# Kernel optimization log

Measured on AMD Instinct MI355X. Metric: run time of the kernel, lower is better.

The kernel has to match this reference:

```python
import jax, jax.numpy as jnp
import numpy as np

B, D, E, H, DEPTH, NH, K = 4, 384, 8, 1536, 12, 6, 2
P, NTOK = 16, 197  # patch size, 14*14 patches + cls
EPS = 1e-6


def layernorm(x, w, b):
    m = x.mean(-1, keepdims=True)
    v = ((x - m) ** 2).mean(-1, keepdims=True)
    return (x - m) / jnp.sqrt(v + EPS) * w + b


def attention(x, qkv_w, qkv_b, proj_w, proj_b):
    Bn, N, C = x.shape
    hd = C // NH
    qkv = x @ qkv_w.T + qkv_b                       # [B,N,3C]
    qkv = qkv.reshape(Bn, N, 3, NH, hd).transpose(2, 0, 3, 1, 4)
    q, k, v = qkv[0], qkv[1], qkv[2]                # [B,h,N,hd]
    attn = jax.nn.softmax((q @ k.transpose(0, 1, 3, 2)) * (hd ** -0.5), axis=-1)
    out = (attn @ v).transpose(0, 2, 1, 3).reshape(Bn, N, C)
    return out @ proj_w.T + proj_b


def mlp(x, w1, b1, w2, b2):
    h = jax.nn.gelu(x @ w1.T + b1, approximate=False)
    return h @ w2.T + b2


def moe_ffn(x2d, gw, w1, b1, w2, b2):
    # noiseless top-k gating (eval mode of NoisyTopKGating)
    logits = x2d @ gw                                # [T,E]
    T = logits.shape[0]
    top_vals, top_idx = jax.lax.top_k(logits, K + 1)
    gates_k = jax.nn.softmax(top_vals[:, :K], axis=-1)
    gates = jnp.zeros((T, E), x2d.dtype).at[jnp.arange(T)[:, None], top_idx[:, :K]].set(gates_k)
    # dense per-expert FFN, weighted combine (identical math to SparseDispatcher)
    h = jax.nn.gelu(jnp.einsum('td,edh->teh', x2d, w1) + b1, approximate=False)
    out = jnp.einsum('teh,ehd->ted', h, w2) + b2
    return jnp.einsum('te,ted->td', gates, out)


def forward(x, patch_w, patch_b, cls_token, pos_embed,
            ln1_w, ln1_b, qkv_w, qkv_b, proj_w, proj_b, ln2_w, ln2_b,
            fc1_w, fc1_b, fc2_w, fc2_b,
            gate_w, moe_w1, moe_b1, moe_w2, moe_b2, lnf_w, lnf_b):
    # patch embed: conv k=16 s=16
    feat = jax.lax.conv_general_dilated(x, patch_w, (P, P), 'VALID',
                                        dimension_numbers=('NCHW', 'OIHW', 'NCHW'))
    feat = feat + patch_b[None, :, None, None]
    Bn = feat.shape[0]
    tokens = feat.reshape(Bn, D, -1).transpose(0, 2, 1)          # [B,196,D]
    cls = jnp.broadcast_to(cls_token, (Bn, 1, D))
    h = jnp.concatenate([cls, tokens], axis=1) + pos_embed       # [B,197,D]

    for i in range(DEPTH):
        h = h + attention(layernorm(h, ln1_w[i], ln1_b[i]), qkv_w[i], qkv_b[i], proj_w[i], proj_b[i])
        y = layernorm(h, ln2_w[i], ln2_b[i])
        if i % 2 == 1:
            j = i // 2
            y2 = moe_ffn(y.reshape(-1, D), gate_w[j], moe_w1[j], moe_b1[j], moe_w2[j], moe_b2[j])
            h = h + y2.reshape(Bn, NTOK, D)
        else:
            j = i // 2
            h = h + mlp(y, fc1_w[j], fc1_b[j], fc2_w[j], fc2_b[j])
    return layernorm(h, lnf_w, lnf_b)


def setup_inputs() -> dict:
    key = jax.random.key(0)
    ks = jax.random.split(key, 16)
    rn = lambda k, s, sd=0.02: jax.random.normal(k, s, jnp.float32) * sd
    return {
        'x': jax.random.normal(ks[0], (B, 3, 224, 224), jnp.float32),
        'patch_w': rn(ks[1], (D, 3, P, P)), 'patch_b': jnp.zeros((D,), jnp.float32),
        'cls_token': rn(ks[2], (1, 1, D)), 'pos_embed': rn(ks[3], (1, NTOK, D)),
        'ln1_w': jnp.ones((DEPTH, D), jnp.float32), 'ln1_b': jnp.zeros((DEPTH, D), jnp.float32),
        'qkv_w': rn(ks[4], (DEPTH, 3 * D, D)), 'qkv_b': jnp.zeros((DEPTH, 3 * D), jnp.float32),
        'proj_w': rn(ks[5], (DEPTH, D, D)), 'proj_b': jnp.zeros((DEPTH, D), jnp.float32),
        'ln2_w': jnp.ones((DEPTH, D), jnp.float32), 'ln2_b': jnp.zeros((DEPTH, D), jnp.float32),
        'fc1_w': rn(ks[6], (DEPTH // 2, H, D)), 'fc1_b': jnp.zeros((DEPTH // 2, H), jnp.float32),
        'fc2_w': rn(ks[7], (DEPTH // 2, D, H)), 'fc2_b': jnp.zeros((DEPTH // 2, D), jnp.float32),
        'gate_w': rn(ks[8], (DEPTH // 2, D, E)),
        'moe_w1': rn(ks[9], (DEPTH // 2, E, D, H)), 'moe_b1': jnp.zeros((DEPTH // 2, E, H), jnp.float32),
        'moe_w2': rn(ks[10], (DEPTH // 2, E, H, D)), 'moe_b2': jnp.zeros((DEPTH // 2, E, D), jnp.float32),
        'lnf_w': jnp.ones((D,), jnp.float32), 'lnf_b': jnp.zeros((D,), jnp.float32),
    }


def reference(x, patch_w, patch_b, cls_token, pos_embed,
              ln1_w, ln1_b, qkv_w, qkv_b, proj_w, proj_b, ln2_w, ln2_b,
              fc1_w, fc1_b, fc2_w, fc2_b,
              gate_w, moe_w1, moe_b1, moe_w2, moe_b2, lnf_w, lnf_b):
    return forward(x, patch_w, patch_b, cls_token, pos_embed,
                   ln1_w, ln1_b, qkv_w, qkv_b, proj_w, proj_b, ln2_w, ln2_b,
                   fc1_w, fc1_b, fc2_w, fc2_b,
                   gate_w, moe_w1, moe_b1, moe_w2, moe_b2, lnf_w, lnf_b)
```

## Files before the change

kernel.cpp:

```cpp
#include <hip/hip_runtime.h>
#include <math.h>

#define NBATCH 4
#define NTOK 197
#define TT 788
#define DM 384
#define HM 1536
#define NHEAD 6
#define NEXP 8
#define LD2 72
#define MOUTSZ (TT * 2 * DM)

typedef __attribute__((ext_vector_type(8))) short bf16x8;
typedef __attribute__((ext_vector_type(4))) float f32x4;

__device__ __forceinline__ void f2bf2(float x, short& hi, short& lo) {
    unsigned u = __float_as_uint(x);
    unsigned uh = u + (0x7fffu + ((u >> 16) & 1u));
    hi = (short)(uh >> 16);
    float hf = __uint_as_float(uh & 0xffff0000u);
    float r = x - hf;
    unsigned v = __float_as_uint(r);
    lo = (short)((v + (0x7fffu + ((v >> 16) & 1u))) >> 16);
}
__device__ __forceinline__ float gelu_f(float x) {
    return 0.5f * x * (1.0f + erff(x * 0.7071067811865475f));
}

__global__ void k_im2col(const float* __restrict__ X, float* __restrict__ P) {
    int p = blockIdx.x;
    int b = p / 196, pp = p % 196;
    int py = pp / 14, px = pp % 14;
    const float* xb = X + (size_t)b * 3 * 224 * 224;
    float* dst = P + (size_t)p * 768;
    for (int idx = threadIdx.x; idx < 768; idx += 256) {
        int c = idx >> 8;
        int i = (idx >> 4) & 15;
        int j = idx & 15;
        dst[idx] = xb[((size_t)c * 224 + py * 16 + i) * 224 + px * 16 + j];
    }
}

__global__ void k_assemble(const float* __restrict__ PO, const float* __restrict__ pb,
                           const float* __restrict__ cls, const float* __restrict__ pos,
                           float* __restrict__ H) {
    int t = blockIdx.x;
    int b = t / NTOK, n = t % NTOK;
    for (int d = threadIdx.x; d < DM; d += 128) {
        float v;
        if (n == 0) v = cls[d];
        else v = PO[((size_t)b * 196 + (n - 1)) * DM + d] + pb[d];
        H[(size_t)t * DM + d] = v + pos[(size_t)n * DM + d];
    }
}

__global__ void k_ln(const float* __restrict__ X, const float* __restrict__ w,
                     const float* __restrict__ b, float* __restrict__ Y) {
    int t = blockIdx.x, lane = threadIdx.x;
    const float* x = X + (size_t)t * DM;
    float v[6];
    float s = 0.f;
    #pragma unroll
    for (int i = 0; i < 6; ++i) { v[i] = x[lane + i * 64]; s += v[i]; }
    #pragma unroll
    for (int off = 32; off; off >>= 1) s += __shfl_xor(s, off);
    float mean = s * (1.f / 384.f);
    float q = 0.f;
    #pragma unroll
    for (int i = 0; i < 6; ++i) { float d = v[i] - mean; q += d * d; }
    #pragma unroll
    for (int off = 32; off; off >>= 1) q += __shfl_xor(q, off);
    float inv = rsqrtf(q * (1.f / 384.f) + 1e-6f);
    float* y = Y + (size_t)t * DM;
    #pragma unroll
    for (int i = 0; i < 6; ++i) {
        int d = lane + i * 64;
        y[d] = (v[i] - mean) * inv * w[d] + b[d];
    }
}

__global__ __launch_bounds__(256) void k_gemm_mfma(
    const float* __restrict__ A, const float* __restrict__ W,
    const float* __restrict__ bias, float* __restrict__ C,
    int M, int N, int K, int flags, int MT, int NT, int wprot, int ksplit,
    const float* __restrict__ lnw, const float* __restrict__ lnb)
{
    int mt, nt, ks = 0;
    {
        int lane8 = blockIdx.x & 7;
        int idx = blockIdx.x >> 3;
        if (ksplit > 1) { ks = idx % ksplit; idx /= ksplit; }
        if (wprot) {
            mt = idx % MT;
            nt = lane8 + 8 * (idx / MT);
            if (nt >= NT) return;
        } else {
            nt = idx % NT;
            mt = lane8 + 8 * (idx / NT);
            if (mt >= MT) return;
        }
    }
    const int Ks = K / ksplit;
    const float* Ab = A + (size_t)ks * Ks;
    const float* Wb = W + (size_t)ks * Ks;
    __shared__ short Ah[64 * LD2], Al[64 * LD2], Bh[64 * LD2], Bl[64 * LD2];
    const int bm = mt * 64, bn = nt * 64;
    const int tid = threadIdx.x;
    const int lane = tid & 63, w = tid >> 6;
    const int wr = w >> 1, wc = w & 1;
    const int r16 = lane & 15, g = lane >> 4;
    const int sr = tid >> 4;
    const int sc = (tid & 15) * 4;
    const bool doln = (flags & 8) != 0;
    float am[4], ai[4];
    #pragma unroll
    for (int p = 0; p < 4; ++p) { am[p] = 0.f; ai[p] = 1.f; }
    if (doln) {
        int j = tid & 15;
        #pragma unroll
        for (int p = 0; p < 4; ++p) {
            int r = bm + sr + p * 16;
            if (r < M) {
                const float* xr = A + (size_t)r * K;
                float s = 0.f, ss = 0.f;
                #pragma unroll
                for (int i = 0; i < 6; ++i) {
                    float4 v = *(const float4*)(xr + j * 4 + i * 64);
                    s += v.x + v.y + v.z + v.w;
                    ss += v.x * v.x + v.y * v.y + v.z * v.z + v.w * v.w;
                }
                #pragma unroll
                for (int off = 1; off < 16; off <<= 1) {
                    s += __shfl_xor(s, off);
                    ss += __shfl_xor(ss, off);
                }
                float mean = s * (1.f / 384.f);
                float var = ss * (1.f / 384.f) - mean * mean;
                am[p] = mean;
                ai[p] = rsqrtf(var + 1e-6f);
            }
        }
    }
    float4 ra[4], rb[4], lw4, lb4;
    auto LOADT = [&](int k0) {
        if (doln) {
            lw4 = *(const float4*)(lnw + k0 + sc);
            lb4 = *(const float4*)(lnb + k0 + sc);
        }
        #pragma unroll
        for (int p = 0; p < 4; ++p) {
            int r = sr + p * 16;
            ra[p] = make_float4(0.f, 0.f, 0.f, 0.f);
            if (bm + r < M) ra[p] = *(const float4*)(Ab + (size_t)(bm + r) * K + k0 + sc);
            rb[p] = *(const float4*)(Wb + (size_t)(bn + r) * K + k0 + sc);
        }
    };
    auto STORET = [&]() {
        #pragma unroll
        for (int p = 0; p < 4; ++p) {
            int r = sr + p * 16;
            float4 a4 = ra[p];
            if (doln) {
                a4.x = (a4.x - am[p]) * ai[p] * lw4.x + lb4.x;
                a4.y = (a4.y - am[p]) * ai[p] * lw4.y + lb4.y;
                a4.z = (a4.z - am[p]) * ai[p] * lw4.z + lb4.z;
                a4.w = (a4.w - am[p]) * ai[p] * lw4.w + lb4.w;
            }
            float4 b4 = rb[p];
            short4 ah, al, bh, bl;
            f2bf2(a4.x, ah.x, al.x); f2bf2(a4.y, ah.y, al.y);
            f2bf2(a4.z, ah.z, al.z); f2bf2(a4.w, ah.w, al.w);
            f2bf2(b4.x, bh.x, bl.x); f2bf2(b4.y, bh.y, bl.y);
            f2bf2(b4.z, bh.z, bl.z); f2bf2(b4.w, bh.w, bl.w);
            *(short4*)&Ah[r * LD2 + sc] = ah; *(short4*)&Al[r * LD2 + sc] = al;
            *(short4*)&Bh[r * LD2 + sc] = bh; *(short4*)&Bl[r * LD2 + sc] = bl;
        }
    };
    f32x4 acc[2][2] = {};
    auto COMPUTE = [&]() {
        #pragma unroll
        for (int kk = 0; kk < 2; ++kk) {
            bf16x8 afh[2], afl[2], bfh[2], bfl[2];
            #pragma unroll
            for (int i = 0; i < 2; ++i) {
                int off = (wr * 32 + i * 16 + r16) * LD2 + kk * 32 + g * 8;
                afh[i] = *(const bf16x8*)&Ah[off];
                afl[i] = *(const bf16x8*)&Al[off];
            }
            #pragma unroll
            for (int j = 0; j < 2; ++j) {
                int off = (wc * 32 + j * 16 + r16) * LD2 + kk * 32 + g * 8;
                bfh[j] = *(const bf16x8*)&Bh[off];
                bfl[j] = *(const bf16x8*)&Bl[off];
            }
            #pragma unroll
            for (int i = 0; i < 2; ++i)
                #pragma unroll
                for (int j = 0; j < 2; ++j) {
                    acc[i][j] = __builtin_amdgcn_mfma_f32_16x16x32_bf16(afl[i], bfh[j], acc[i][j], 0, 0, 0);
                    acc[i][j] = __builtin_amdgcn_mfma_f32_16x16x32_bf16(afh[i], bfl[j], acc[i][j], 0, 0, 0);
                    acc[i][j] = __builtin_amdgcn_mfma_f32_16x16x32_bf16(afh[i], bfh[j], acc[i][j], 0, 0, 0);
                }
        }
    };
    LOADT(0);
    STORET();
    __syncthreads();
    for (int k0 = 64; k0 < Ks; k0 += 64) {
        LOADT(k0);
        COMPUTE();
        __syncthreads();
        STORET();
        __syncthreads();
    }
    COMPUTE();
    #pragma unroll
    for (int i = 0; i < 2; ++i) {
        #pragma unroll
        for (int j = 0; j < 2; ++j) {
            int n = bn + wc * 32 + j * 16 + r16;
            float bb = (bias && ks == 0) ? bias[n] : 0.f;
            int mbase = bm + wr * 32 + i * 16 + g * 4;
            #pragma unroll
            for (int r = 0; r < 4; ++r) {
                int m = mbase + r;
                if (m < M) {
                    float v = acc[i][j][r] + bb;
                    float* cp = C + (size_t)m * N + n;
                    if (flags & 16) {
                        atomicAdd(cp, v);
                    } else {
                        if (flags & 1) v = gelu_f(v);
                        if (flags & 2) v += *cp;
                        *cp = v;
                    }
                }
            }
        }
    }
}

__global__ __launch_bounds__(256) void k_gemm32(
    const float* __restrict__ A, const float* __restrict__ W,
    const float* __restrict__ bias, float* __restrict__ C,
    int M, int N, int K, int flags, int MT, int NT,
    const float* __restrict__ lnw, const float* __restrict__ lnb)
{
    int mt, nt;
    {
        int lane8 = blockIdx.x & 7;
        int idx = blockIdx.x >> 3;
        mt = idx % MT;
        nt = lane8 + 8 * (idx / MT);
        if (nt >= NT) return;
    }
    __shared__ short Ah[32 * LD2], Al[32 * LD2], Bh[64 * LD2], Bl[64 * LD2];
    const int bm = mt * 32, bn = nt * 64;
    const int tid = threadIdx.x;
    const int lane = tid & 63, w = tid >> 6;
    const int r16 = lane & 15, g = lane >> 4;
    const int sa = tid >> 3;
    const int ja = tid & 7;
    const int sca = ja * 8;
    const int sr = tid >> 4;
    const int sc = (tid & 15) * 4;
    const bool doln = (flags & 8) != 0;
    const bool dogelu = (flags & 1) != 0;
    const int rowA = bm + sa;
    const bool aok = rowA < M;
    float am = 0.f, ai = 1.f;
    if (doln && aok) {
        const float* xr = A + (size_t)rowA * K;
        float s = 0.f, ss = 0.f;
        #pragma unroll
        for (int i = 0; i < 12; ++i) {
            float4 v = *(const float4*)(xr + ja * 48 + i * 4);
            s += v.x + v.y + v.z + v.w;
            ss += v.x * v.x + v.y * v.y + v.z * v.z + v.w * v.w;
        }
        #pragma unroll
        for (int off = 1; off < 8; off <<= 1) {
            s += __shfl_xor(s, off);
            ss += __shfl_xor(ss, off);
        }
        float mean = s * (1.f / 384.f);
        float var = ss * (1.f / 384.f) - mean * mean;
        am = mean;
        ai = rsqrtf(var + 1e-6f);
    }
    float4 ra0, ra1, rb[4], lwa0, lwa1, lba0, lba1;
    auto LOADT = [&](int k0) {
        if (doln) {
            lwa0 = *(const float4*)(lnw + k0 + sca);
            lwa1 = *(const float4*)(lnw + k0 + sca + 4);
            lba0 = *(const float4*)(lnb + k0 + sca);
            lba1 = *(const float4*)(lnb + k0 + sca + 4);
        }
        ra0 = make_float4(0.f, 0.f, 0.f, 0.f);
        ra1 = ra0;
        if (aok) {
            ra0 = *(const float4*)(A + (size_t)rowA * K + k0 + sca);
            ra1 = *(const float4*)(A + (size_t)rowA * K + k0 + sca + 4);
        }
        #pragma unroll
        for (int p = 0; p < 4; ++p) {
            int r = sr + p * 16;
            rb[p] = *(const float4*)(W + (size_t)(bn + r) * K + k0 + sc);
        }
    };
    auto STORET = [&]() {
        float4 a0 = ra0, a1 = ra1;
        if (doln) {
            a0.x = (a0.x - am) * ai * lwa0.x + lba0.x;
            a0.y = (a0.y - am) * ai * lwa0.y + lba0.y;
            a0.z = (a0.z - am) * ai * lwa0.z + lba0.z;
            a0.w = (a0.w - am) * ai * lwa0.w + lba0.w;
            a1.x = (a1.x - am) * ai * lwa1.x + lba1.x;
            a1.y = (a1.y - am) * ai * lwa1.y + lba1.y;
            a1.z = (a1.z - am) * ai * lwa1.z + lba1.z;
            a1.w = (a1.w - am) * ai * lwa1.w + lba1.w;
        }
        short4 h0, l0, h1, l1;
        f2bf2(a0.x, h0.x, l0.x); f2bf2(a0.y, h0.y, l0.y);
        f2bf2(a0.z, h0.z, l0.z); f2bf2(a0.w, h0.w, l0.w);
        f2bf2(a1.x, h1.x, l1.x); f2bf2(a1.y, h1.y, l1.y);
        f2bf2(a1.z, h1.z, l1.z); f2bf2(a1.w, h1.w, l1.w);
        *(short4*)&Ah[sa * LD2 + sca] = h0; *(short4*)&Ah[sa * LD2 + sca + 4] = h1;
        *(short4*)&Al[sa * LD2 + sca] = l0; *(short4*)&Al[sa * LD2 + sca + 4] = l1;
        #pragma unroll
        for (int p = 0; p < 4; ++p) {
            int r = sr + p * 16;
            float4 b4 = rb[p];
            short4 bh, bl;
            f2bf2(b4.x, bh.x, bl.x); f2bf2(b4.y, bh.y, bl.y);
            f2bf2(b4.z, bh.z, bl.z); f2bf2(b4.w, bh.w, bl.w);
            *(short4*)&Bh[r * LD2 + sc] = bh; *(short4*)&Bl[r * LD2 + sc] = bl;
        }
    };
    f32x4 acc[2] = {};
    auto COMPUTE = [&]() {
        #pragma unroll
        for (int kk = 0; kk < 2; ++kk) {
            bf16x8 afh[2], afl[2], bfh, bfl;
            #pragma unroll
            for (int i = 0; i < 2; ++i) {
                int off = (i * 16 + r16) * LD2 + kk * 32 + g * 8;
                afh[i] = *(const bf16x8*)&Ah[off];
                afl[i] = *(const bf16x8*)&Al[off];
            }
            {
                int off = (w * 16 + r16) * LD2 + kk * 32 + g * 8;
                bfh = *(const bf16x8*)&Bh[off];
                bfl = *(const bf16x8*)&Bl[off];
            }
            #pragma unroll
            for (int i = 0; i < 2; ++i) {
                acc[i] = __builtin_amdgcn_mfma_f32_16x16x32_bf16(afl[i], bfh, acc[i], 0, 0, 0);
                acc[i] = __builtin_amdgcn_mfma_f32_16x16x32_bf16(afh[i], bfl, acc[i], 0, 0, 0);
                acc[i] = __builtin_amdgcn_mfma_f32_16x16x32_bf16(afh[i], bfh, acc[i], 0, 0, 0);
            }
        }
    };
    LOADT(0);
    STORET();
    __syncthreads();
    for (int k0 = 64; k0 < K; k0 += 64) {
        LOADT(k0);
        COMPUTE();
        __syncthreads();
        STORET();
        __syncthreads();
    }
    COMPUTE();
    #pragma unroll
    for (int i = 0; i < 2; ++i) {
        int n = bn + w * 16 + r16;
        float bb = bias ? bias[n] : 0.f;
        int mbase = bm + i * 16 + g * 4;
        #pragma unroll
        for (int r = 0; r < 4; ++r) {
            int m = mbase + r;
            if (m < M) {
                float v = acc[i][r] + bb;
                if (dogelu) v = gelu_f(v);
                C[(size_t)m * N + n] = v;
            }
        }
    }
}

__global__ __launch_bounds__(256) void k_scoresm(const float* __restrict__ QKV,
                                                 float* __restrict__ S) {
    int z = blockIdx.y;
    int b = z / NHEAD, hh = z % NHEAD;
    int i0 = blockIdx.x * 32;
    __shared__ float qs[32][65];
    __shared__ float ks[32][65];
    __shared__ float srow[32][200];
    int tid = threadIdx.x;
    int r = tid >> 3, d0 = (tid & 7) * 8, c0 = (tid & 7) * 4, l8 = tid & 7;
    {
        float4 v0 = make_float4(0,0,0,0), v1 = v0;
        if (i0 + r < NTOK) {
            const float* qp = QKV + ((size_t)(b * NTOK + i0 + r)) * 1152 + hh * 64 + d0;
            v0 = *(const float4*)qp; v1 = *(const float4*)(qp + 4);
        }
        qs[r][d0+0]=v0.x; qs[r][d0+1]=v0.y; qs[r][d0+2]=v0.z; qs[r][d0+3]=v0.w;
        qs[r][d0+4]=v1.x; qs[r][d0+5]=v1.y; qs[r][d0+6]=v1.z; qs[r][d0+7]=v1.w;
    }
    if (l8 == 0) { srow[r][197] = -1e30f; srow[r][198] = -1e30f; srow[r][199] = -1e30f; }
    for (int j0 = 0; j0 < NTOK; j0 += 32) {
        __syncthreads();
        {
            float4 v0 = make_float4(0,0,0,0), v1 = v0;
            if (j0 + r < NTOK) {
                const float* kp = QKV + ((size_t)(b * NTOK + j0 + r)) * 1152 + 384 + hh * 64 + d0;
                v0 = *(const float4*)kp; v1 = *(const float4*)(kp + 4);
            }
            ks[r][d0+0]=v0.x; ks[r][d0+1]=v0.y; ks[r][d0+2]=v0.z; ks[r][d0+3]=v0.w;
            ks[r][d0+4]=v1.x; ks[r][d0+5]=v1.y; ks[r][d0+6]=v1.z; ks[r][d0+7]=v1.w;
        }
        __syncthreads();
        float acc[4] = {0.f, 0.f, 0.f, 0.f};
        #pragma unroll 8
        for (int d = 0; d < 64; ++d) {
            float qv = qs[r][d];
            #pragma unroll
            for (int u = 0; u < 4; ++u) acc[u] += qv * ks[c0 + u][d];
        }
        #pragma unroll
        for (int u = 0; u < 4; ++u) {
            int j = j0 + c0 + u;
            if (j < NTOK) srow[r][j] = acc[u] * 0.125f;
        }
    }
    __syncthreads();
    float m = -1e30f;
    for (int c = l8; c < 200; c += 8) m = fmaxf(m, srow[r][c]);
    #pragma unroll
    for (int off = 1; off < 8; off <<= 1) m = fmaxf(m, __shfl_xor(m, off));
    float s = 0.f;
    for (int c = l8; c < 200; c += 8) {
        float e = expf(srow[r][c] - m);
        srow[r][c] = e;
        s += e;
    }
    #pragma unroll
    for (int off = 1; off < 8; off <<= 1) s += __shfl_xor(s, off);
    float invs = 1.f / s;
    int i = i0 + r;
    if (i < NTOK) {
        float* sp = S + ((size_t)z * NTOK + i) * NTOK;
        for (int c = l8; c < NTOK; c += 8) sp[c] = srow[r][c] * invs;
    }
}

__global__ __launch_bounds__(256) void k_pv(const float* __restrict__ S, const float* __restrict__ QKV,
                                            float* __restrict__ AO) {
    int z = blockIdx.y;
    int b = z / NHEAD, hh = z % NHEAD;
    int i0 = blockIdx.x * 32;
    __shared__ float ps[32][33];
    __shared__ float vs[32][65];
    int tid = threadIdx.x;
    int r = tid >> 3;
    int c4 = (tid & 7) * 4;
    int d0 = (tid & 7) * 8;
    float acc[8] = {};
    for (int k0 = 0; k0 < NTOK; k0 += 32) {
        #pragma unroll
        for (int u = 0; u < 4; ++u) {
            int i = i0 + r, j = k0 + c4 + u;
            ps[r][c4 + u] = (i < NTOK && j < NTOK) ? S[((size_t)z * NTOK + i) * NTOK + j] : 0.f;
        }
        {
            float4 v0 = make_float4(0,0,0,0), v1 = v0;
            if (k0 + r < NTOK) {
                const float* vp = QKV + ((size_t)(b * NTOK + k0 + r)) * 1152 + 768 + hh * 64 + d0;
                v0 = *(const float4*)vp; v1 = *(const float4*)(vp + 4);
            }
            vs[r][d0+0]=v0.x; vs[r][d0+1]=v0.y; vs[r][d0+2]=v0.z; vs[r][d0+3]=v0.w;
            vs[r][d0+4]=v1.x; vs[r][d0+5]=v1.y; vs[r][d0+6]=v1.z; vs[r][d0+7]=v1.w;
        }
        __syncthreads();
        #pragma unroll 8
        for (int kk = 0; kk < 32; ++kk) {
            float pw = ps[r][kk];
            #pragma unroll
            for (int j = 0; j < 8; ++j) acc[j] += pw * vs[kk][d0 + j];
        }
        __syncthreads();
    }
    int i = i0 + r;
    if (i < NTOK) {
        float* op = AO + (size_t)(b * NTOK + i) * DM + hh * 64 + d0;
        #pragma unroll
        for (int j = 0; j < 8; ++j) op[j] = acc[j];
    }
}

__global__ void k_route_ln(const float* __restrict__ H, float* __restrict__ lnstat,
                           const float* __restrict__ lnw, const float* __restrict__ lnb,
                           const float* __restrict__ GW,
                           int* __restrict__ eidx, float* __restrict__ egate) {
    int t = blockIdx.x * 4 + (threadIdx.x >> 6);
    if (t >= TT) return;
    int lane = threadIdx.x & 63;
    const float* x = H + (size_t)t * DM;
    float v[6];
    float s = 0.f, ss = 0.f;
    #pragma unroll
    for (int i = 0; i < 6; ++i) {
        v[i] = x[lane + i * 64];
        s += v[i];
        ss += v[i] * v[i];
    }
    #pragma unroll
    for (int off = 32; off; off >>= 1) { s += __shfl_xor(s, off); ss += __shfl_xor(ss, off); }
    float mean = s * (1.f / 384.f);
    float var = ss * (1.f / 384.f) - mean * mean;
    float inv = rsqrtf(var + 1e-6f);
    if (lane == 0) { lnstat[2 * t] = mean; lnstat[2 * t + 1] = inv; }
    float l8v[NEXP] = {};
    #pragma unroll
    for (int i = 0; i < 6; ++i) {
        int d = lane + i * 64;
        float yv = (v[i] - mean) * inv * lnw[d] + lnb[d];
        const float* g = GW + (size_t)d * NEXP;
        #pragma unroll
        for (int e = 0; e < NEXP; ++e) l8v[e] += yv * g[e];
    }
    #pragma unroll
    for (int e = 0; e < NEXP; ++e) {
        float vv = l8v[e];
        #pragma unroll
        for (int off = 32; off; off >>= 1) vv += __shfl_xor(vv, off);
        l8v[e] = vv;
    }
    if (lane == 0) {
        int b0 = 0;
        #pragma unroll
        for (int e = 1; e < NEXP; ++e) if (l8v[e] > l8v[b0]) b0 = e;
        int b1 = -1;
        #pragma unroll
        for (int e = 0; e < NEXP; ++e) if (e != b0 && (b1 < 0 || l8v[e] > l8v[b1])) b1 = e;
        float e1 = expf(l8v[b1] - l8v[b0]);
        float denom = 1.f + e1;
        eidx[2 * t] = b0; eidx[2 * t + 1] = b1;
        egate[2 * t] = 1.f / denom; egate[2 * t + 1] = e1 / denom;
    }
}

__global__ void k_pscatter(int* __restrict__ cnt, int* __restrict__ basep,
                           const int* __restrict__ eidx,
                           int* __restrict__ slot_tok, int* __restrict__ slot_of) {
    __shared__ int hist[NEXP];
    __shared__ int bp[NEXP];
    __shared__ int fl[NEXP];
    int tid = threadIdx.x;
    if (tid < NEXP) { hist[tid] = 0; fl[tid] = 0; }
    __syncthreads();
    for (int i = tid; i < 2 * TT; i += 256) atomicAdd(&hist[eidx[i]], 1);
    __syncthreads();
    if (tid == 0) {
        int s = 0;
        for (int e = 0; e < NEXP; ++e) { bp[e] = s; s += hist[e]; }
    }
    __syncthreads();
    if (tid < NEXP) { cnt[tid] = hist[tid]; basep[tid] = bp[tid]; }
    for (int t = tid; t < TT; t += 256) {
        #pragma unroll
        for (int k = 0; k < 2; ++k) {
            int e = eidx[2 * t + k];
            int pos = atomicAdd(&fl[e], 1);
            int s = bp[e] + pos;
            slot_tok[s] = t;
            slot_of[2 * t + k] = s;
        }
    }
}

__global__ __launch_bounds__(256) void k_moe1_mfma(
    const float* __restrict__ H, const float* __restrict__ lnstat,
    const float* __restrict__ lnw, const float* __restrict__ lnb,
    const float* __restrict__ W1, const float* __restrict__ B1,
    const int* __restrict__ slot_tok, const int* __restrict__ cnt, const int* __restrict__ basep,
    float* __restrict__ HID)
{
    const int e = blockIdx.x & 7;
    const int idx = blockIdx.x >> 3;
    const int mt = idx % 13;
    const int nt = idx / 13;
    const int c = cnt[e];
    const int r0 = mt * 64;
    if (r0 >= c) return;
    const int sbase = basep[e];
    const int n0 = nt * 64;
    const float* W = W1 + (size_t)e * DM * HM;
    const float* B1e = B1 + (size_t)e * HM;
    __shared__ short Ah[64 * LD2], Al[64 * LD2], Bh[64 * LD2], Bl[64 * LD2];
    const int tid = threadIdx.x;
    const int lane = tid & 63, w = tid >> 6;
    const int wr = w >> 1, wc = w & 1;
    const int r16 = lane & 15, g = lane >> 4;
    const int sr = tid >> 4, sc = (tid & 15) * 4;
    const int kq = (tid >> 4) * 4;
    int tokp[4];
    float am4[4], ai4[4];
    #pragma unroll
    for (int p = 0; p < 4; ++p) {
        int m = r0 + sr + p * 16;
        tokp[p] = (m < c) ? slot_tok[sbase + m] : -1;
        am4[p] = 0.f; ai4[p] = 1.f;
        if (tokp[p] >= 0) { am4[p] = lnstat[2 * tokp[p]]; ai4[p] = lnstat[2 * tokp[p] + 1]; }
    }
    f32x4 acc[2][2] = {};
    for (int k0 = 0; k0 < DM; k0 += 64) {
        float4 lw4 = *(const float4*)(lnw + k0 + sc);
        float4 lb4 = *(const float4*)(lnb + k0 + sc);
        #pragma unroll
        for (int p = 0; p < 4; ++p) {
            int r = sr + p * 16;
            float4 a4 = make_float4(0.f, 0.f, 0.f, 0.f);
            if (tokp[p] >= 0) {
                a4 = *(const float4*)(H + (size_t)tokp[p] * DM + k0 + sc);
                a4.x = (a4.x - am4[p]) * ai4[p] * lw4.x + lb4.x;
                a4.y = (a4.y - am4[p]) * ai4[p] * lw4.y + lb4.y;
                a4.z = (a4.z - am4[p]) * ai4[p] * lw4.z + lb4.z;
                a4.w = (a4.w - am4[p]) * ai4[p] * lw4.w + lb4.w;
            }
            short4 ah, al;
            f2bf2(a4.x, ah.x, al.x); f2bf2(a4.y, ah.y, al.y);
            f2bf2(a4.z, ah.z, al.z); f2bf2(a4.w, ah.w, al.w);
            *(short4*)&Ah[r * LD2 + sc] = ah; *(short4*)&Al[r * LD2 + sc] = al;
        }
        {
            float4 b4[4];
            #pragma unroll
            for (int i = 0; i < 4; ++i)
                b4[i] = *(const float4*)(W + (size_t)(k0 + kq + i) * HM + n0 + sc);
            float col[4][4] = {
                { b4[0].x, b4[1].x, b4[2].x, b4[3].x },
                { b4[0].y, b4[1].y, b4[2].y, b4[3].y },
                { b4[0].z, b4[1].z, b4[2].z, b4[3].z },
                { b4[0].w, b4[1].w, b4[2].w, b4[3].w } };
            #pragma unroll
            for (int u = 0; u < 4; ++u) {
                short4 hh, ll;
                f2bf2(col[u][0], hh.x, ll.x); f2bf2(col[u][1], hh.y, ll.y);
                f2bf2(col[u][2], hh.z, ll.z); f2bf2(col[u][3], hh.w, ll.w);
                *(short4*)&Bh[(sc + u) * LD2 + kq] = hh;
                *(short4*)&Bl[(sc + u) * LD2 + kq] = ll;
            }
        }
        __syncthreads();
        #pragma unroll
        for (int kk = 0; kk < 2; ++kk) {
            bf16x8 afh[2], afl[2], bfh[2], bfl[2];
            #pragma unroll
            for (int i = 0; i < 2; ++i) {
                int off = (wr * 32 + i * 16 + r16) * LD2 + kk * 32 + g * 8;
                afh[i] = *(const bf16x8*)&Ah[off];
                afl[i] = *(const bf16x8*)&Al[off];
            }
            #pragma unroll
            for (int j = 0; j < 2; ++j) {
                int off = (wc * 32 + j * 16 + r16) * LD2 + kk * 32 + g * 8;
                bfh[j] = *(const bf16x8*)&Bh[off];
                bfl[j] = *(const bf16x8*)&Bl[off];
            }
            #pragma unroll
            for (int i = 0; i < 2; ++i)
                #pragma unroll
                for (int j = 0; j < 2; ++j) {
                    acc[i][j] = __builtin_amdgcn_mfma_f32_16x16x32_bf16(afl[i], bfh[j], acc[i][j], 0, 0, 0);
                    acc[i][j] = __builtin_amdgcn_mfma_f32_16x16x32_bf16(afh[i], bfl[j], acc[i][j], 0, 0, 0);
                    acc[i][j] = __builtin_amdgcn_mfma_f32_16x16x32_bf16(afh[i], bfh[j], acc[i][j], 0, 0, 0);
                }
        }
        __syncthreads();
    }
    #pragma unroll
    for (int i = 0; i < 2; ++i) {
        #pragma unroll
        for (int j = 0; j < 2; ++j) {
            int n = n0 + wc * 32 + j * 16 + r16;
            float bb = B1e[n];
            #pragma unroll
            for (int r = 0; r < 4; ++r) {
                int m = r0 + wr * 32 + i * 16 + g * 4 + r;
                if (m < c)
                    HID[(size_t)(sbase + m) * HM + n] = gelu_f(acc[i][j][r] + bb);
            }
        }
    }
}

__global__ __launch_bounds__(256) void k_moe2_mfma(
    const float* __restrict__ HID, const float* __restrict__ W2,
    const int* __restrict__ cnt, const int* __restrict__ basep,
    float* __restrict__ MOUTP)
{
    const int e = blockIdx.x & 7;
    const int idx = blockIdx.x >> 3;
    const int mt = idx % 13;
    const int rest = idx / 13;
    const int nt = rest % 6;
    const int ks = rest / 6;
    const int c = cnt[e];
    const int r0 = mt * 64;
    if (r0 >= c) return;
    const int sbase = basep[e];
    const int n0 = nt * 64;
    const int kbase = ks * 384;
    const float* W = W2 + (size_t)e * HM * DM + (size_t)kbase * DM;
    float* outp = MOUTP + (size_t)ks * MOUTSZ;
    __shared__ short Ah[64 * LD2], Al[64 * LD2], Bh[64 * LD2], Bl[64 * LD2];
    const int tid = threadIdx.x;
    const int lane = tid & 63, w = tid >> 6;
    const int wr = w >> 1, wc = w & 1;
    const int r16 = lane & 15, g = lane >> 4;
    const int sr = tid >> 4, sc = (tid & 15) * 4;
    const int kq = (tid >> 4) * 4;
    f32x4 acc[2][2] = {};
    for (int k0 = 0; k0 < 384; k0 += 64) {
        #pragma unroll
        for (int p = 0; p < 4; ++p) {
            int r = sr + p * 16;
            int m = r0 + r;
            float4 a4 = make_float4(0.f, 0.f, 0.f, 0.f);
            if (m < c) a4 = *(const float4*)(HID + (size_t)(sbase + m) * HM + kbase + k0 + sc);
            short4 ah, al;
            f2bf2(a4.x, ah.x, al.x); f2bf2(a4.y, ah.y, al.y);
            f2bf2(a4.z, ah.z, al.z); f2bf2(a4.w, ah.w, al.w);
            *(short4*)&Ah[r * LD2 + sc] = ah; *(short4*)&Al[r * LD2 + sc] = al;
        }
        {
            float4 b4[4];
            #pragma unroll
            for (int i = 0; i < 4; ++i)
                b4[i] = *(const float4*)(W + (size_t)(k0 + kq + i) * DM + n0 + sc);
            float col[4][4] = {
                { b4[0].x, b4[1].x, b4[2].x, b4[3].x },
                { b4[0].y, b4[1].y, b4[2].y, b4[3].y },
                { b4[0].z, b4[1].z, b4[2].z, b4[3].z },
                { b4[0].w, b4[1].w, b4[2].w, b4[3].w } };
            #pragma unroll
            for (int u = 0; u < 4; ++u) {
                short4 hh, ll;
                f2bf2(col[u][0], hh.x, ll.x); f2bf2(col[u][1], hh.y, ll.y);
                f2bf2(col[u][2], hh.z, ll.z); f2bf2(col[u][3], hh.w, ll.w);
                *(short4*)&Bh[(sc + u) * LD2 + kq] = hh;
                *(short4*)&Bl[(sc + u) * LD2 + kq] = ll;
            }
        }
        __syncthreads();
        #pragma unroll
        for (int kk = 0; kk < 2; ++kk) {
            bf16x8 afh[2], afl[2], bfh[2], bfl[2];
            #pragma unroll
            for (int i = 0; i < 2; ++i) {
                int off = (wr * 32 + i * 16 + r16) * LD2 + kk * 32 + g * 8;
                afh[i] = *(const bf16x8*)&Ah[off];
                afl[i] = *(const bf16x8*)&Al[off];
            }
            #pragma unroll
            for (int j = 0; j < 2; ++j) {
                int off = (wc * 32 + j * 16 + r16) * LD2 + kk * 32 + g * 8;
                bfh[j] = *(const bf16x8*)&Bh[off];
                bfl[j] = *(const bf16x8*)&Bl[off];
            }
            #pragma unroll
            for (int i = 0; i < 2; ++i)
                #pragma unroll
                for (int j = 0; j < 2; ++j) {
                    acc[i][j] = __builtin_amdgcn_mfma_f32_16x16x32_bf16(afl[i], bfh[j], acc[i][j], 0, 0, 0);
                    acc[i][j] = __builtin_amdgcn_mfma_f32_16x16x32_bf16(afh[i], bfl[j], acc[i][j], 0, 0, 0);
                    acc[i][j] = __builtin_amdgcn_mfma_f32_16x16x32_bf16(afh[i], bfh[j], acc[i][j], 0, 0, 0);
                }
        }
        __syncthreads();
    }
    #pragma unroll
    for (int i = 0; i < 2; ++i) {
        #pragma unroll
        for (int j = 0; j < 2; ++j) {
            int n = n0 + wc * 32 + j * 16 + r16;
            #pragma unroll
            for (int r = 0; r < 4; ++r) {
                int m = r0 + wr * 32 + i * 16 + g * 4 + r;
                if (m < c)
                    outp[(size_t)(sbase + m) * DM + n] = acc[i][j][r];
            }
        }
    }
}

__global__ void k_combine(const float* __restrict__ MOUTP, const int* __restrict__ slot_of,
                          const int* __restrict__ eidx, const float* __restrict__ egate,
                          const float* __restrict__ B2, float* __restrict__ H) {
    int t = blockIdx.x;
    int s0 = slot_of[2 * t], s1 = slot_of[2 * t + 1];
    int e0 = eidx[2 * t], e1 = eidx[2 * t + 1];
    float g0 = egate[2 * t], g1 = egate[2 * t + 1];
    for (int d = threadIdx.x; d < DM; d += 128) {
        float v0 = B2[(size_t)e0 * DM + d];
        float v1 = B2[(size_t)e1 * DM + d];
        #pragma unroll
        for (int p = 0; p < 4; ++p) {
            v0 += MOUTP[(size_t)p * MOUTSZ + (size_t)s0 * DM + d];
            v1 += MOUTP[(size_t)p * MOUTSZ + (size_t)s1 * DM + d];
        }
        H[(size_t)t * DM + d] += g0 * v0 + g1 * v1;
    }
}

extern "C" void kernel_launch(void* const* d_in, const int* in_sizes, int n_in,
                              void* d_out, int out_size, void* d_ws, size_t ws_size,
                              hipStream_t stream) {
    const float* x         = (const float*)d_in[0];
    const float* patch_w   = (const float*)d_in[1];
    const float* patch_b   = (const float*)d_in[2];
    const float* cls_token = (const float*)d_in[3];
    const float* pos_embed = (const float*)d_in[4];
    const float* ln1_w     = (const float*)d_in[5];
    const float* ln1_b     = (const float*)d_in[6];
    const float* qkv_w     = (const float*)d_in[7];
    const float* qkv_b     = (const float*)d_in[8];
    const float* proj_w    = (const float*)d_in[9];
    const float* proj_b    = (const float*)d_in[10];
    const float* ln2_w     = (const float*)d_in[11];
    const float* ln2_b     = (const float*)d_in[12];
    const float* fc1_w     = (const float*)d_in[13];
    const float* fc1_b     = (const float*)d_in[14];
    const float* fc2_w     = (const float*)d_in[15];
    const float* fc2_b     = (const float*)d_in[16];
    const float* gate_w    = (const float*)d_in[17];
    const float* moe_w1    = (const float*)d_in[18];
    const float* moe_b1    = (const float*)d_in[19];
    const float* moe_w2    = (const float*)d_in[20];
    const float* moe_b2    = (const float*)d_in[21];
    const float* lnf_w     = (const float*)d_in[22];
    const float* lnf_b     = (const float*)d_in[23];
    float* out = (float*)d_out;

    float* wsf = (float*)d_ws;
    float* regA     = wsf;
    float* patches  = regA;
    float* patchout = regA + 602112;
    float* moehid   = regA;
    float* h     = regA + 2420736;
    float* spare = h + 302592;
    float* qkvb  = spare + 302592;
    float* attno = qkvb + 907776;
    float* regC  = attno + 302592;
    float* S    = regC;
    float* hid  = regC;
    float* mout4 = qkvb;
    float* egate = regC + 1210368;
    int* ib       = (int*)(egate + 1576);
    int* eidx     = ib;
    int* slot_tok = ib + 1576;
    int* slot_of  = ib + 3152;
    int* cnt      = ib + 4728;
    int* basep    = ib + 4736;
    float* lnstat = (float*)(ib + 4752);

    k_im2col<<<784, 256, 0, stream>>>(x, patches);
    k_gemm_mfma<<<96, 256, 0, stream>>>(patches, patch_w, nullptr, patchout,
                                        784, DM, 768, 0, 13, 6, 0, 1, nullptr, nullptr);
    k_assemble<<<TT, 128, 0, stream>>>(patchout, patch_b, cls_token, pos_embed, h);

    for (int l = 0; l < 12; ++l) {
        k_gemm32<<<600, 256, 0, stream>>>(h, qkv_w + (size_t)l * 1152 * DM,
                                          qkv_b + l * 1152, qkvb, TT, 1152, DM, 8,
                                          25, 18, ln1_w + l * DM, ln1_b + l * DM);
        k_scoresm<<<dim3(7, NBATCH * NHEAD), 256, 0, stream>>>(qkvb, S);
        k_pv<<<dim3(7, NBATCH * NHEAD), 256, 0, stream>>>(S, qkvb, attno);
        k_gemm_mfma<<<192, 256, 0, stream>>>(attno, proj_w + (size_t)l * DM * DM,
                                             proj_b + l * DM, h, TT, DM, DM, 16,
                                             13, 6, 0, 2, nullptr, nullptr);
        int j = l >> 1;
        if ((l & 1) == 0) {
            k_gemm32<<<600, 256, 0, stream>>>(h, fc1_w + (size_t)j * HM * DM,
                                              fc1_b + j * HM, hid, TT, HM, DM, 9,
                                              25, 24, ln2_w + l * DM, ln2_b + l * DM);
            k_gemm_mfma<<<384, 256, 0, stream>>>(hid, fc2_w + (size_t)j * DM * HM,
                                                 fc2_b + j * DM, h, TT, DM, HM, 16,
                                                 13, 6, 0, 4, nullptr, nullptr);
        } else {
            k_route_ln<<<197, 256, 0, stream>>>(h, lnstat, ln2_w + l * DM, ln2_b + l * DM,
                                                gate_w + (size_t)j * DM * NEXP, eidx, egate);
            k_pscatter<<<1, 256, 0, stream>>>(cnt, basep, eidx, slot_tok, slot_of);
            k_moe1_mfma<<<8 * 13 * 24, 256, 0, stream>>>(
                h, lnstat, ln2_w + l * DM, ln2_b + l * DM,
                moe_w1 + (size_t)j * NEXP * DM * HM, moe_b1 + (size_t)j * NEXP * HM,
                slot_tok, cnt, basep, moehid);
            k_moe2_mfma<<<8 * 13 * 24, 256, 0, stream>>>(
                moehid, moe_w2 + (size_t)j * NEXP * HM * DM, cnt, basep, mout4);
            k_combine<<<TT, 128, 0, stream>>>(mout4, slot_of, eidx, egate,
                                              moe_b2 + (size_t)j * NEXP * DM, h);
        }
    }
    k_ln<<<TT, 64, 0, stream>>>(h, lnf_w, lnf_b, out);
}
```

Measured before the change: 1.633 ms.

## Use 32-row M tiles and register-prefetch pipelining in MoE expert GEMMs

Both MoE expert GEMM kernels drop the M tile from 64 to 32 rows, going from 13 to 25 M-tiles per expert. Each wave now owns a 16-column N slice across all 32 rows. The main loop is restructured to load the next K tile's global data into registers while MFMAs run on the current shared-memory tile, overlapping global latency with compute. Smaller tiles waste fewer rows on the uneven per-expert token counts and launch more useful blocks, at the cost of reloading weight tiles more often and more early-exiting blocks.

New measurement: 1.678 ms. 1.03x slower.

```diff
diff --git a/kernel.cpp b/kernel.cpp
--- a/kernel.cpp
+++ b/kernel.cpp
@@ -580,7 +580,7 @@
     }
 }
 
-__global__ __launch_bounds__(256) void k_moe1_mfma(
+__global__ __launch_bounds__(256) void k_moe1_32(
     const float* __restrict__ H, const float* __restrict__ lnstat,
     const float* __restrict__ lnw, const float* __restrict__ lnb,
     const float* __restrict__ W1, const float* __restrict__ B1,
@@ -589,209 +589,233 @@
 {
     const int e = blockIdx.x & 7;
     const int idx = blockIdx.x >> 3;
-    const int mt = idx % 13;
-    const int nt = idx / 13;
+    const int mt = idx % 25;
+    const int nt = idx / 25;
     const int c = cnt[e];
-    const int r0 = mt * 64;
+    const int r0 = mt * 32;
     if (r0 >= c) return;
     const int sbase = basep[e];
     const int n0 = nt * 64;
     const float* W = W1 + (size_t)e * DM * HM;
     const float* B1e = B1 + (size_t)e * HM;
-    __shared__ short Ah[64 * LD2], Al[64 * LD2], Bh[64 * LD2], Bl[64 * LD2];
+    __shared__ short Ah[32 * LD2], Al[32 * LD2], Bh[64 * LD2], Bl[64 * LD2];
     const int tid = threadIdx.x;
     const int lane = tid & 63, w = tid >> 6;
-    const int wr = w >> 1, wc = w & 1;
     const int r16 = lane & 15, g = lane >> 4;
-    const int sr = tid >> 4, sc = (tid & 15) * 4;
+    const int sa = tid >> 3;
+    const int ja = tid & 7;
+    const int sca = ja * 8;
+    const int sc = (tid & 15) * 4;
     const int kq = (tid >> 4) * 4;
-    int tokp[4];
-    float am4[4], ai4[4];
-    #pragma unroll
-    for (int p = 0; p < 4; ++p) {
-        int m = r0 + sr + p * 16;
-        tokp[p] = (m < c) ? slot_tok[sbase + m] : -1;
-        am4[p] = 0.f; ai4[p] = 1.f;
-        if (tokp[p] >= 0) { am4[p] = lnstat[2 * tokp[p]]; ai4[p] = lnstat[2 * tokp[p] + 1]; }
-    }
-    f32x4 acc[2][2] = {};
-    for (int k0 = 0; k0 < DM; k0 += 64) {
-        float4 lw4 = *(const float4*)(lnw + k0 + sc);
-        float4 lb4 = *(const float4*)(lnb + k0 + sc);
-        #pragma unroll
-        for (int p = 0; p < 4; ++p) {
-            int r = sr + p * 16;
-            float4 a4 = make_float4(0.f, 0.f, 0.f, 0.f);
-            if (tokp[p] >= 0) {
-                a4 = *(const float4*)(H + (size_t)tokp[p] * DM + k0 + sc);
-                a4.x = (a4.x - am4[p]) * ai4[p] * lw4.x + lb4.x;
-                a4.y = (a4.y - am4[p]) * ai4[p] * lw4.y + lb4.y;
-                a4.z = (a4.z - am4[p]) * ai4[p] * lw4.z + lb4.z;
-                a4.w = (a4.w - am4[p]) * ai4[p] * lw4.w + lb4.w;
-            }
-            short4 ah, al;
-            f2bf2(a4.x, ah.x, al.x); f2bf2(a4.y, ah.y, al.y);
-            f2bf2(a4.z, ah.z, al.z); f2bf2(a4.w, ah.w, al.w);
-            *(short4*)&Ah[r * LD2 + sc] = ah; *(short4*)&Al[r * LD2 + sc] = al;
-        }
-        {
-            float4 b4[4];
-            #pragma unroll
-            for (int i = 0; i < 4; ++i)
-                b4[i] = *(const float4*)(W + (size_t)(k0 + kq + i) * HM + n0 + sc);
-            float col[4][4] = {
-                { b4[0].x, b4[1].x, b4[2].x, b4[3].x },
-                { b4[0].y, b4[1].y, b4[2].y, b4[3].y },
-                { b4[0].z, b4[1].z, b4[2].z, b4[3].z },
-                { b4[0].w, b4[1].w, b4[2].w, b4[3].w } };
-            #pragma unroll
-            for (int u = 0; u < 4; ++u) {
-                short4 hh, ll;
-                f2bf2(col[u][0], hh.x, ll.x); f2bf2(col[u][1], hh.y, ll.y);
-                f2bf2(col[u][2], hh.z, ll.z); f2bf2(col[u][3], hh.w, ll.w);
-                *(short4*)&Bh[(sc + u) * LD2 + kq] = hh;
-                *(short4*)&Bl[(sc + u) * LD2 + kq] = ll;
-            }
-        }
-        __syncthreads();
+    int mrow = r0 + sa;
+    int tok = (mrow < c) ? slot_tok[sbase + mrow] : -1;
+    float am = 0.f, ai = 1.f;
+    if (tok >= 0) { am = lnstat[2 * tok]; ai = lnstat[2 * tok + 1]; }
+    float4 ra0, ra1, rbw[4], lwa0, lwa1, lba0, lba1;
+    auto LOADT = [&](int k0) {
+        lwa0 = *(const float4*)(lnw + k0 + sca);
+        lwa1 = *(const float4*)(lnw + k0 + sca + 4);
+        lba0 = *(const float4*)(lnb + k0 + sca);
+        lba1 = *(const float4*)(lnb + k0 + sca + 4);
+        ra0 = make_float4(0.f, 0.f, 0.f, 0.f);
+        ra1 = ra0;
+        if (tok >= 0) {
+            ra0 = *(const float4*)(H + (size_t)tok * DM + k0 + sca);
+            ra1 = *(const float4*)(H + (size_t)tok * DM + k0 + sca + 4);
+        }
+        #pragma unroll
+        for (int i = 0; i < 4; ++i)
+            rbw[i] = *(const float4*)(W + (size_t)(k0 + kq + i) * HM + n0 + sc);
+    };
+    auto STORET = [&]() {
+        float4 a0 = ra0, a1 = ra1;
+        a0.x = (a0.x - am) * ai * lwa0.x + lba0.x;
+        a0.y = (a0.y - am) * ai * lwa0.y + lba0.y;
+        a0.z = (a0.z - am) * ai * lwa0.z + lba0.z;
+        a0.w = (a0.w - am) * ai * lwa0.w + lba0.w;
+        a1.x = (a1.x - am) * ai * lwa1.x + lba1.x;
+        a1.y = (a1.y - am) * ai * lwa1.y + lba1.y;
+        a1.z = (a1.z - am) * ai * lwa1.z + lba1.z;
+        a1.w = (a1.w - am) * ai * lwa1.w + lba1.w;
+        short4 h0, l0, h1, l1;
+        f2bf2(a0.x, h0.x, l0.x); f2bf2(a0.y, h0.y, l0.y);
+        f2bf2(a0.z, h0.z, l0.z); f2bf2(a0.w, h0.w, l0.w);
+        f2bf2(a1.x, h1.x, l1.x); f2bf2(a1.y, h1.y, l1.y);
+        f2bf2(a1.z, h1.z, l1.z); f2bf2(a1.w, h1.w, l1.w);
+        *(short4*)&Ah[sa * LD2 + sca] = h0; *(short4*)&Ah[sa * LD2 + sca + 4] = h1;
+        *(short4*)&Al[sa * LD2 + sca] = l0; *(short4*)&Al[sa * LD2 + sca + 4] = l1;
+        float col[4][4] = {
+            { rbw[0].x, rbw[1].x, rbw[2].x, rbw[3].x },
+            { rbw[0].y, rbw[1].y, rbw[2].y, rbw[3].y },
+            { rbw[0].z, rbw[1].z, rbw[2].z, rbw[3].z },
+            { rbw[0].w, rbw[1].w, rbw[2].w, rbw[3].w } };
+        #pragma unroll
+        for (int u = 0; u < 4; ++u) {
+            short4 hh, ll;
+            f2bf2(col[u][0], hh.x, ll.x); f2bf2(col[u][1], hh.y, ll.y);
+            f2bf2(col[u][2], hh.z, ll.z); f2bf2(col[u][3], hh.w, ll.w);
+            *(short4*)&Bh[(sc + u) * LD2 + kq] = hh;
+            *(short4*)&Bl[(sc + u) * LD2 + kq] = ll;
+        }
+    };
+    f32x4 acc[2] = {};
+    auto COMPUTE = [&]() {
         #pragma unroll
         for (int kk = 0; kk < 2; ++kk) {
-            bf16x8 afh[2], afl[2], bfh[2], bfl[2];
+            bf16x8 afh[2], afl[2], bfh, bfl;
             #pragma unroll
             for (int i = 0; i < 2; ++i) {
-                int off = (wr * 32 + i * 16 + r16) * LD2 + kk * 32 + g * 8;
+                int off = (i * 16 + r16) * LD2 + kk * 32 + g * 8;
                 afh[i] = *(const bf16x8*)&Ah[off];
                 afl[i] = *(const bf16x8*)&Al[off];
             }
-            #pragma unroll
-            for (int j = 0; j < 2; ++j) {
-                int off = (wc * 32 + j * 16 + r16) * LD2 + kk * 32 + g * 8;
-                bfh[j] = *(const bf16x8*)&Bh[off];
-                bfl[j] = *(const bf16x8*)&Bl[off];
-            }
-            #pragma unroll
-            for (int i = 0; i < 2; ++i)
-                #pragma unroll
-                for (int j = 0; j < 2; ++j) {
-                    acc[i][j] = __builtin_amdgcn_mfma_f32_16x16x32_bf16(afl[i], bfh[j], acc[i][j], 0, 0, 0);
-                    acc[i][j] = __builtin_amdgcn_mfma_f32_16x16x32_bf16(afh[i], bfl[j], acc[i][j], 0, 0, 0);
-                    acc[i][j] = __builtin_amdgcn_mfma_f32_16x16x32_bf16(afh[i], bfh[j], acc[i][j], 0, 0, 0);
-                }
-        }
-        __syncthreads();
-    }
+            {
+                int off = (w * 16 + r16) * LD2 + kk * 32 + g * 8;
+                bfh = *(const bf16x8*)&Bh[off];
+                bfl = *(const bf16x8*)&Bl[off];
+            }
+            #pragma unroll
+            for (int i = 0; i < 2; ++i) {
+                acc[i] = __builtin_amdgcn_mfma_f32_16x16x32_bf16(afl[i], bfh, acc[i], 0, 0, 0);
+                acc[i] = __builtin_amdgcn_mfma_f32_16x16x32_bf16(afh[i], bfl, acc[i], 0, 0, 0);
+                acc[i] = __builtin_amdgcn_mfma_f32_16x16x32_bf16(afh[i], bfh, acc[i], 0, 0, 0);
+            }
+        }
+    };
+    LOADT(0);
+    STORET();
+    __syncthreads();
+    for (int k0 = 64; k0 < DM; k0 += 64) {
+        LOADT(k0);
+        COMPUTE();
+        __syncthreads();
+        STORET();
+        __syncthreads();
+    }
+    COMPUTE();
     #pragma unroll
     for (int i = 0; i < 2; ++i) {
-        #pragma unroll
-        for (int j = 0; j < 2; ++j) {
-            int n = n0 + wc * 32 + j * 16 + r16;
-            float bb = B1e[n];
-            #pragma unroll
-            for (int r = 0; r < 4; ++r) {
-                int m = r0 + wr * 32 + i * 16 + g * 4 + r;
-                if (m < c)
-                    HID[(size_t)(sbase + m) * HM + n] = gelu_f(acc[i][j][r] + bb);
-            }
-        }
-    }
-}
-
-__global__ __launch_bounds__(256) void k_moe2_mfma(
+        int n = n0 + w * 16 + r16;
+        float bb = B1e[n];
+        int mbase = r0 + i * 16 + g * 4;
+        #pragma unroll
+        for (int r = 0; r < 4; ++r) {
+            int m = mbase + r;
+            if (m < c)
+                HID[(size_t)(sbase + m) * HM + n] = gelu_f(acc[i][r] + bb);
+        }
+    }
+}
+
+__global__ __launch_bounds__(256) void k_moe2_32(
     const float* __restrict__ HID, const float* __restrict__ W2,
     const int* __restrict__ cnt, const int* __restrict__ basep,
     float* __restrict__ MOUTP)
 {
     const int e = blockIdx.x & 7;
     const int idx = blockIdx.x >> 3;
-    const int mt = idx % 13;
-    const int rest = idx / 13;
+    const int mt = idx % 25;
+    const int rest = idx / 25;
     const int nt = rest % 6;
     const int ks = rest / 6;
     const int c = cnt[e];
-    const int r0 = mt * 64;
+    const int r0 = mt * 32;
     if (r0 >= c) return;
     const int sbase = basep[e];
     const int n0 = nt * 64;
     const int kbase = ks * 384;
     const float* W = W2 + (size_t)e * HM * DM + (size_t)kbase * DM;
     float* outp = MOUTP + (size_t)ks * MOUTSZ;
-    __shared__ short Ah[64 * LD2], Al[64 * LD2], Bh[64 * LD2], Bl[64 * LD2];
+    __shared__ short Ah[32 * LD2], Al[32 * LD2], Bh[64 * LD2], Bl[64 * LD2];
     const int tid = threadIdx.x;
     const int lane = tid & 63, w = tid >> 6;
-    const int wr = w >> 1, wc = w & 1;
     const int r16 = lane & 15, g = lane >> 4;
-    const int sr = tid >> 4, sc = (tid & 15) * 4;
+    const int sa = tid >> 3;
+    const int ja = tid & 7;
+    const int sca = ja * 8;
+    const int sc = (tid & 15) * 4;
     const int kq = (tid >> 4) * 4;
-    f32x4 acc[2][2] = {};
-    for (int k0 = 0; k0 < 384; k0 += 64) {
-        #pragma unroll
-        for (int p = 0; p < 4; ++p) {
-            int r = sr + p * 16;
-            int m = r0 + r;
-            float4 a4 = make_float4(0.f, 0.f, 0.f, 0.f);
-            if (m < c) a4 = *(const float4*)(HID + (size_t)(sbase + m) * HM + kbase + k0 + sc);
-            short4 ah, al;
-            f2bf2(a4.x, ah.x, al.x); f2bf2(a4.y, ah.y, al.y);
-            f2bf2(a4.z, ah.z, al.z); f2bf2(a4.w, ah.w, al.w);
-            *(short4*)&Ah[r * LD2 + sc] = ah; *(short4*)&Al[r * LD2 + sc] = al;
-        }
-        {
-            float4 b4[4];
-            #pragma unroll
-            for (int i = 0; i < 4; ++i)
-                b4[i] = *(const float4*)(W + (size_t)(k0 + kq + i) * DM + n0 + sc);
-            float col[4][4] = {
-                { b4[0].x, b4[1].x, b4[2].x, b4[3].x },
-                { b4[0].y, b4[1].y, b4[2].y, b4[3].y },
-                { b4[0].z, b4[1].z, b4[2].z, b4[3].z },
-                { b4[0].w, b4[1].w, b4[2].w, b4[3].w } };
-            #pragma unroll
-            for (int u = 0; u < 4; ++u) {
-                short4 hh, ll;
-                f2bf2(col[u][0], hh.x, ll.x); f2bf2(col[u][1], hh.y, ll.y);
-                f2bf2(col[u][2], hh.z, ll.z); f2bf2(col[u][3], hh.w, ll.w);
-                *(short4*)&Bh[(sc + u) * LD2 + kq] = hh;
-                *(short4*)&Bl[(sc + u) * LD2 + kq] = ll;
-            }
-        }
-        __syncthreads();
+    int mrow = r0 + sa;
+    const bool aok = mrow < c;
+    const float* ap = HID + (size_t)(sbase + mrow) * HM + kbase;
+    float4 ra0, ra1, rbw[4];
+    auto LOADT = [&](int k0) {
+        ra0 = make_float4(0.f, 0.f, 0.f, 0.f);
+        ra1 = ra0;
+        if (aok) {
+            ra0 = *(const float4*)(ap + k0 + sca);
+            ra1 = *(const float4*)(ap + k0 + sca + 4);
+        }
+        #pragma unroll
+        for (int i = 0; i < 4; ++i)
+            rbw[i] = *(const float4*)(W + (size_t)(k0 + kq + i) * DM + n0 + sc);
+    };
+    auto STORET = [&]() {
+        short4 h0, l0, h1, l1;
+        f2bf2(ra0.x, h0.x, l0.x); f2bf2(ra0.y, h0.y, l0.y);
+        f2bf2(ra0.z, h0.z, l0.z); f2bf2(ra0.w, h0.w, l0.w);
+        f2bf2(ra1.x, h1.x, l1.x); f2bf2(ra1.y, h1.y, l1.y);
+        f2bf2(ra1.z, h1.z, l1.z); f2bf2(ra1.w, h1.w, l1.w);
+        *(short4*)&Ah[sa * LD2 + sca] = h0; *(short4*)&Ah[sa * LD2 + sca + 4] = h1;
+        *(short4*)&Al[sa * LD2 + sca] = l0; *(short4*)&Al[sa * LD2 + sca + 4] = l1;
+        float col[4][4] = {
+            { rbw[0].x, rbw[1].x, rbw[2].x, rbw[3].x },
+            { rbw[0].y, rbw[1].y, rbw[2].y, rbw[3].y },
+            { rbw[0].z, rbw[1].z, rbw[2].z, rbw[3].z },
+            { rbw[0].w, rbw[1].w, rbw[2].w, rbw[3].w } };
+        #pragma unroll
+        for (int u = 0; u < 4; ++u) {
+            short4 hh, ll;
+            f2bf2(col[u][0], hh.x, ll.x); f2bf2(col[u][1], hh.y, ll.y);
+            f2bf2(col[u][2], hh.z, ll.z); f2bf2(col[u][3], hh.w, ll.w);
+            *(short4*)&Bh[(sc + u) * LD2 + kq] = hh;
+            *(short4*)&Bl[(sc + u) * LD2 + kq] = ll;
+        }
+    };
+    f32x4 acc[2] = {};
+    auto COMPUTE = [&]() {
         #pragma unroll
         for (int kk = 0; kk < 2; ++kk) {
-            bf16x8 afh[2], afl[2], bfh[2], bfl[2];
+            bf16x8 afh[2], afl[2], bfh, bfl;
             #pragma unroll
             for (int i = 0; i < 2; ++i) {
-                int off = (wr * 32 + i * 16 + r16) * LD2 + kk * 32 + g * 8;
+                int off = (i * 16 + r16) * LD2 + kk * 32 + g * 8;
                 afh[i] = *(const bf16x8*)&Ah[off];
                 afl[i] = *(const bf16x8*)&Al[off];
             }
-            #pragma unroll
-            for (int j = 0; j < 2; ++j) {
-                int off = (wc * 32 + j * 16 + r16) * LD2 + kk * 32 + g * 8;
-                bfh[j] = *(const bf16x8*)&Bh[off];
-                bfl[j] = *(const bf16x8*)&Bl[off];
-            }
-            #pragma unroll
-            for (int i = 0; i < 2; ++i)
-                #pragma unroll
-                for (int j = 0; j < 2; ++j) {
-                    acc[i][j] = __builtin_amdgcn_mfma_f32_16x16x32_bf16(afl[i], bfh[j], acc[i][j], 0, 0, 0);
-                    acc[i][j] = __builtin_amdgcn_mfma_f32_16x16x32_bf16(afh[i], bfl[j], acc[i][j], 0, 0, 0);
-                    acc[i][j] = __builtin_amdgcn_mfma_f32_16x16x32_bf16(afh[i], bfh[j], acc[i][j], 0, 0, 0);
-                }
-        }
-        __syncthreads();
-    }
+            {
+                int off = (w * 16 + r16) * LD2 + kk * 32 + g * 8;
+                bfh = *(const bf16x8*)&Bh[off];
+                bfl = *(const bf16x8*)&Bl[off];
+            }
+            #pragma unroll
+            for (int i = 0; i < 2; ++i) {
+                acc[i] = __builtin_amdgcn_mfma_f32_16x16x32_bf16(afl[i], bfh, acc[i], 0, 0, 0);
+                acc[i] = __builtin_amdgcn_mfma_f32_16x16x32_bf16(afh[i], bfl, acc[i], 0, 0, 0);
+                acc[i] = __builtin_amdgcn_mfma_f32_16x16x32_bf16(afh[i], bfh, acc[i], 0, 0, 0);
+            }
+        }
+    };
+    LOADT(0);
+    STORET();
+    __syncthreads();
+    for (int k0 = 64; k0 < 384; k0 += 64) {
+        LOADT(k0);
+        COMPUTE();
+        __syncthreads();
+        STORET();
+        __syncthreads();
+    }
+    COMPUTE();
     #pragma unroll
     for (int i = 0; i < 2; ++i) {
-        #pragma unroll
-        for (int j = 0; j < 2; ++j) {
-            int n = n0 + wc * 32 + j * 16 + r16;
-            #pragma unroll
-            for (int r = 0; r < 4; ++r) {
-                int m = r0 + wr * 32 + i * 16 + g * 4 + r;
-                if (m < c)
-                    outp[(size_t)(sbase + m) * DM + n] = acc[i][j][r];
-            }
+        int n = n0 + w * 16 + r16;
+        int mbase = r0 + i * 16 + g * 4;
+        #pragma unroll
+        for (int r = 0; r < 4; ++r) {
+            int m = mbase + r;
+            if (m < c)
+                outp[(size_t)(sbase + m) * DM + n] = acc[i][r];
         }
     }
 }
@@ -892,11 +916,11 @@
             k_route_ln<<<197, 256, 0, stream>>>(h, lnstat, ln2_w + l * DM, ln2_b + l * DM,
                                                 gate_w + (size_t)j * DM * NEXP, eidx, egate);
             k_pscatter<<<1, 256, 0, stream>>>(cnt, basep, eidx, slot_tok, slot_of);
-            k_moe1_mfma<<<8 * 13 * 24, 256, 0, stream>>>(
+            k_moe1_32<<<8 * 25 * 24, 256, 0, stream>>>(
                 h, lnstat, ln2_w + l * DM, ln2_b + l * DM,
                 moe_w1 + (size_t)j * NEXP * DM * HM, moe_b1 + (size_t)j * NEXP * HM,
                 slot_tok, cnt, basep, moehid);
-            k_moe2_mfma<<<8 * 13 * 24, 256, 0, stream>>>(
+            k_moe2_32<<<8 * 25 * 24, 256, 0, stream>>>(
                 moehid, moe_w2 + (size_t)j * NEXP * HM * DM, cnt, basep, mout4);
             k_combine<<<TT, 128, 0, stream>>>(mout4, slot_of, eidx, egate,
                                               moe_b2 + (size_t)j * NEXP * DM, h);
```
